# Optimization experiments

Hardware: AMD Instinct MI355X
Metric: run time of the kernel (lower is better)

## Reference

```python
import jax, jax.numpy as jnp
import numpy as np

B, T, D, H = 4, 2048, 768, 12
HD = D // H  # head size 64
DF = 3072    # feed-forward size


def setup_inputs() -> dict:
    key = jax.random.key(0)
    ks = jax.random.split(key, 10)
    s = 0.02
    return {
        "x": jax.random.normal(ks[0], (B, T, D), jnp.float32),
        "mask": jnp.ones((B, T), jnp.int32),
        "Wq": jax.random.normal(ks[1], (D, D), jnp.float32) * s,
        "bq": jnp.zeros((D,), jnp.float32),
        "Wk": jax.random.normal(ks[2], (D, D), jnp.float32) * s,
        "bk": jnp.zeros((D,), jnp.float32),
        "Wv": jax.random.normal(ks[3], (D, D), jnp.float32) * s,
        "bv": jnp.zeros((D,), jnp.float32),
        "Wo": jax.random.normal(ks[4], (D, D), jnp.float32) * s,
        "bo": jnp.zeros((D,), jnp.float32),
        "W1": jax.random.normal(ks[5], (D, DF), jnp.float32) * s,
        "b1": jnp.zeros((DF,), jnp.float32),
        "W2": jax.random.normal(ks[6], (DF, D), jnp.float32) * s,
        "b2": jnp.zeros((D,), jnp.float32),
    }


def reference(x, mask, Wq, bq, Wk, bk, Wv, bv, Wo, bo, W1, b1, W2, b2):
    scale = 1.0 / np.sqrt(HD).astype(np.float32)
    # projections -> [B, H, T, HD]
    def split_heads(t):
        return t.reshape(B, T, H, HD).transpose(0, 2, 1, 3)
    q = split_heads(x @ Wq + bq)
    k = split_heads(x @ Wk + bk)
    v = split_heads(x @ Wv + bv)
    # [B, H, T, T] attention scores (materialized, as in the original)
    scores = jnp.einsum('bhqd,bhkd->bhqk', q, k) * scale
    neg_inf = jnp.float32(-jnp.inf)
    scores = jnp.where(mask[:, None, None, :] == 0, neg_inf, scores)
    attn = jax.nn.softmax(scores, axis=-1)
    ctx = jnp.einsum('bhqk,bhkd->bhqd', attn, v)          # [B,H,T,HD]
    ctx = ctx.transpose(0, 2, 1, 3).reshape(B, T, D)       # merge heads
    attn_out = ctx @ Wo + bo
    h = x + attn_out                                       # residual 1 (dropout p=0)
    ff = jax.nn.gelu(h @ W1 + b1, approximate=False) @ W2 + b2
    out = h + ff                                           # residual 2
    return out, attn
```

## Files before the change

### kernel.cpp

```cpp
#include <hip/hip_runtime.h>
#include <hip/hip_bf16.h>
#include <math.h>

typedef unsigned short u16;
typedef __attribute__((ext_vector_type(8))) short short8;
typedef __attribute__((ext_vector_type(4))) float f32x4;

constexpr int Bc = 4, Tt = 2048, Dd = 768, Hh = 12, Hd = 64, Df = 3072;
constexpr int BT = Bc * Tt;

__device__ __forceinline__ u16 f2b(float x) {
  __hip_bfloat16 h = __float2bfloat16(x);
  return *reinterpret_cast<u16*>(&h);
}
__device__ __forceinline__ float gelu_exact(float g) {
  return 0.5f * g * (1.0f + erff(g * 0.70710678118654752440f));
}
__device__ __forceinline__ void gload16(const void* g, void* l) {
  __builtin_amdgcn_global_load_lds(
      (const __attribute__((address_space(1))) unsigned int*)g,
      (__attribute__((address_space(3))) unsigned int*)l, 16, 0, 0);
}

__device__ __forceinline__ void tr_tile(const float* __restrict__ in,
                                        u16* __restrict__ out, int R, int C,
                                        int bx, int by, float* sh) {
  const int tx = threadIdx.x & 31, ty = threadIdx.x >> 5;
  const int r0 = by * 32, c0 = bx * 32;
#pragma unroll
  for (int i = 0; i < 4; ++i)
    sh[(ty + i * 8) * 33 + tx] = in[(size_t)(r0 + ty + i * 8) * C + c0 + tx];
  __syncthreads();
#pragma unroll
  for (int i = 0; i < 4; ++i)
    out[(size_t)(c0 + ty + i * 8) * R + r0 + tx] = f2b(sh[tx * 33 + ty + i * 8]);
}

__global__ __launch_bounds__(256) void prep_all(
    const float* __restrict__ x, const float* __restrict__ Wq,
    const float* __restrict__ Wk, const float* __restrict__ Wv,
    const float* __restrict__ Wo, const float* __restrict__ W1,
    const float* __restrict__ W2, const float* __restrict__ bq,
    const float* __restrict__ bk, const float* __restrict__ bv,
    const int* __restrict__ mask, u16* __restrict__ xb,
    u16* __restrict__ wqkvT, u16* __restrict__ woT, u16* __restrict__ w1T,
    u16* __restrict__ w2T, float* __restrict__ biasc,
    unsigned int* __restrict__ mwords) {
  __shared__ float sh[32 * 33];
  const int s = blockIdx.x;
  if (s < 3072) {
    int i = (s * 256 + threadIdx.x) * 8;
    float4 a = *(const float4*)&x[i];
    float4 b = *(const float4*)&x[i + 4];
    u16 t[8] = {f2b(a.x), f2b(a.y), f2b(a.z), f2b(a.w),
                f2b(b.x), f2b(b.y), f2b(b.z), f2b(b.w)};
    *(uint4*)&xb[i] = *(uint4*)t;
  } else if (s < 3648) {
    int u = s - 3072; tr_tile(Wq, wqkvT, Dd, Dd, u % 24, u / 24, sh);
  } else if (s < 4224) {
    int u = s - 3648; tr_tile(Wk, wqkvT + 768 * Dd, Dd, Dd, u % 24, u / 24, sh);
  } else if (s < 4800) {
    int u = s - 4224; tr_tile(Wv, wqkvT + 1536 * Dd, Dd, Dd, u % 24, u / 24, sh);
  } else if (s < 5376) {
    int u = s - 4800; tr_tile(Wo, woT, Dd, Dd, u % 24, u / 24, sh);
  } else if (s < 7680) {
    int u = s - 5376; tr_tile(W1, w1T, Dd, Df, u % 96, u / 96, sh);
  } else if (s < 9984) {
    int u = s - 7680; tr_tile(W2, w2T, Df, Dd, u % 24, u / 24, sh);
  } else if (s < 9993) {
    int i = (s - 9984) * 256 + threadIdx.x;
    biasc[i] = (i < 768) ? bq[i] : (i < 1536) ? bk[i - 768] : bv[i - 1536];
  } else {
    const int id = threadIdx.x;
    const int b_ = id >> 6, kv0 = (id & 63) * 32;
    unsigned int wbits = 0u;
    for (int j = 0; j < 32; ++j)
      wbits |= (mask[b_ * Tt + kv0 + j] ? 1u : 0u) << j;
    mwords[id] = wbits;
  }
}

template <int MODE>
__global__ __launch_bounds__(256) void mgemm(
    const u16* __restrict__ A, const u16* __restrict__ Bt,
    const float* __restrict__ bias, const float* __restrict__ add,
    void* __restrict__ C0, void* __restrict__ C1, void* __restrict__ C2,
    int K, int N) {
  __shared__ __align__(16) u16 As[2][128 * 32];
  __shared__ __align__(16) u16 Bs[2][128 * 32];
  const int tid = threadIdx.x;
  const int lane = tid & 63, wv = tid >> 6;
  const int m0 = blockIdx.y * 128, n0 = blockIdx.x * 128;
  const int wm = (wv >> 1) * 64, wn = (wv & 1) * 64;

  f32x4 acc[4][4] = {};

#define MG_STAGE(k0_, bf_)                                                    \
  {                                                                           \
    _Pragma("unroll") for (int i_ = 0; i_ < 2; ++i_) {                        \
      const int idx_ = i_ * 256 + tid;                                        \
      const int row_ = idx_ >> 2;                                             \
      const int kc_ = (idx_ & 3) * 8;                                         \
      const u16* ga_;                                                         \
      if constexpr (MODE == 2) {                                              \
        const int m_ = m0 + row_, b_ = m_ >> 11, t_ = m_ & 2047;              \
        const int kk_ = (k0_) + kc_, hd_ = kk_ >> 6, d_ = kk_ & 63;           \
        ga_ = &A[(((size_t)(b_ * Hh + hd_) * Tt + t_) << 6) + d_];            \
      } else {                                                                \
        ga_ = &A[(size_t)(m0 + row_) * K + (k0_) + kc_];                      \
      }                                                                       \
      gload16(ga_, &As[bf_][idx_ * 8]);                                       \
      gload16(&Bt[(size_t)(n0 + row_) * K + (k0_) + kc_], &Bs[bf_][idx_ * 8]);\
    }                                                                         \
  }

  MG_STAGE(0, 0);
  __syncthreads();

  int it = 0;
  for (int k0 = 0; k0 < K; k0 += 32, ++it) {
    const int cur = it & 1;
    if (k0 + 32 < K) MG_STAGE(k0 + 32, cur ^ 1);
    short8 af[4], bfr[4];
#pragma unroll
    for (int i = 0; i < 4; ++i) {
      af[i] = *reinterpret_cast<const short8*>(
          &As[cur][(wm + i * 16 + (lane & 15)) * 32 + (lane >> 4) * 8]);
      bfr[i] = *reinterpret_cast<const short8*>(
          &Bs[cur][(wn + i * 16 + (lane & 15)) * 32 + (lane >> 4) * 8]);
    }
#pragma unroll
    for (int i = 0; i < 4; ++i)
#pragma unroll
      for (int j = 0; j < 4; ++j)
        acc[i][j] = __builtin_amdgcn_mfma_f32_16x16x32_bf16(af[i], bfr[j],
                                                            acc[i][j], 0, 0, 0);
    __syncthreads();
  }
#undef MG_STAGE

  const int lr = (lane >> 4) * 4, lc = lane & 15;
#pragma unroll
  for (int i = 0; i < 4; ++i) {
    const int mbase = m0 + wm + i * 16 + lr;
#pragma unroll
    for (int j = 0; j < 4; ++j) {
      const int col = n0 + wn + j * 16 + lc;
      const float bvs = bias[col];
#pragma unroll
      for (int r = 0; r < 4; ++r) {
        const int m = mbase + r;
        float g = acc[i][j][r] + bvs;
        if constexpr (MODE == 5) {
          const int b = m >> 11, t = m & 2047;
          if (col < 768) {
            const int head = col >> 6, d = col & 63;
            ((u16*)C0)[(((size_t)(b * Hh + head) * Tt + t) << 6) + d] = f2b(g);
          } else if (col < 1536) {
            const int c = col - 768, head = c >> 6, d = c & 63;
            ((u16*)C1)[(((size_t)(b * Hh + head) * Tt + t) << 6) + d] = f2b(g);
          } else {
            const int c = col - 1536, head = c >> 6, d = c & 63;
            ((u16*)C2)[(((size_t)(b * Hh + head) * Hd + d) << 11) + t] = f2b(g);
          }
        } else if constexpr (MODE == 2) {
          g += add[(size_t)m * Dd + col];
          ((float*)C0)[(size_t)m * Dd + col] = g;
          ((u16*)C1)[(size_t)m * Dd + col] = f2b(g);
        } else if constexpr (MODE == 3) {
          ((u16*)C0)[(size_t)m * N + col] = f2b(gelu_exact(g));
        } else {
          g += add[(size_t)m * Dd + col];
          ((float*)C0)[(size_t)m * Dd + col] = g;
        }
      }
    }
  }
}

__global__ __launch_bounds__(256) void attn_fused(
    const u16* __restrict__ qb, const u16* __restrict__ kb,
    const u16* __restrict__ vtb, const unsigned int* __restrict__ mwords,
    float* __restrict__ attn, u16* __restrict__ ctxb) {
  const int bh = blockIdx.y;
  const int b = bh / Hh;
  const int q0 = blockIdx.x * 64;
  const u16* Qg = qb + (size_t)bh * Tt * Hd;
  const u16* Kg = kb + (size_t)bh * Tt * Hd;
  const u16* Vg = vtb + (size_t)bh * Hd * Tt;
  float* attng = attn + (size_t)bh * Tt * Tt;
  u16* ctxg = ctxb + (size_t)bh * Tt * Hd;
  const unsigned int* mwp = mwords + b * 64;

  __shared__ __align__(16) u16 Ks[2][128 * 64];
  __shared__ __align__(16) u16 Vs[64 * 128];
  __shared__ __align__(16) float Pf[64 * 128];

  const int tid = threadIdx.x, lane = tid & 63, wv = tid >> 6;
  const int lc = lane & 15, lg = lane >> 4;
  const int ql = wv * 16 + lc;
  const int qsw = lc & 7;

#define STAGE_K(t, bf)                                                       \
  {                                                                          \
    const int kv0_ = (t) * 128;                                              \
    _Pragma("unroll") for (int w_ = 0; w_ < 4; ++w_) {                       \
      const int p_ = w_ * 256 + tid;                                         \
      const int row_ = p_ >> 3, kc8_ = (p_ & 7) ^ (row_ & 7);                \
      gload16(Kg + (size_t)(kv0_ + row_) * Hd + kc8_ * 8, &Ks[bf][p_ * 8]);  \
    }                                                                        \
  }
#define STAGE_V(t)                                                           \
  {                                                                          \
    const int kv0_ = (t) * 128;                                              \
    _Pragma("unroll") for (int w_ = 0; w_ < 4; ++w_) {                       \
      const int p_ = w_ * 256 + tid;                                         \
      const int d_ = p_ >> 4, pc_ = (p_ & 15) ^ (d_ & 7);                    \
      gload16(Vg + (size_t)d_ * Tt + kv0_ + pc_ * 8, &Vs[p_ * 8]);           \
    }                                                                        \
  }
#define FENCE() asm volatile("" ::: "memory")

  short8 qf[2];
#pragma unroll
  for (int ks = 0; ks < 2; ++ks)
    qf[ks] = *(const short8*)&Qg[(size_t)(q0 + ql) * Hd + ks * 32 + lg * 8];

  float l = 0.f;

  STAGE_K(0, 0);
  for (int t = 0; t < 16; ++t) {
    asm volatile("s_waitcnt vmcnt(0)" ::: "memory");
    __builtin_amdgcn_s_barrier();
    FENCE();
    const int bf = t & 1;
    if (t < 15) STAGE_K(t + 1, bf ^ 1);
    f32x4 s[8] = {};
#pragma unroll
    for (int ks = 0; ks < 2; ++ks) {
      const int ph = (ks * 4 + lg) ^ qsw;
#pragma unroll
      for (int i = 0; i < 8; ++i) {
        const short8 af = *(const short8*)&Ks[bf][(i * 16 + lc) * 64 + ph * 8];
        s[i] = __builtin_amdgcn_mfma_f32_16x16x32_bf16(af, qf[ks], s[i], 0, 0, 0);
      }
    }
    const uint4 mw4 = *(const uint4*)&mwp[t * 4];
    const unsigned int mwa[4] = {mw4.x, mw4.y, mw4.z, mw4.w};
    float ts = 0.f;
#pragma unroll
    for (int i = 0; i < 8; ++i) {
      const unsigned int w = mwa[i >> 1];
#pragma unroll
      for (int r = 0; r < 4; ++r) {
        const float bit = (float)((w >> ((i & 1) * 16 + lg * 4 + r)) & 1u);
        ts += __expf(s[i][r] * 0.125f) * bit;
      }
    }
    ts += __shfl_xor(ts, 16);
    ts += __shfl_xor(ts, 32);
    l += ts;
  }

  const float linv = 1.f / l;
  f32x4 cacc[4] = {};

  __builtin_amdgcn_s_barrier();
  FENCE();

  STAGE_K(0, 0);
  STAGE_V(0);
  for (int t = 0; t < 16; ++t) {
    const int kv0 = t * 128;
    const int bf = t & 1;
    if (t == 0)
      asm volatile("s_waitcnt vmcnt(0)" ::: "memory");
    else
      asm volatile("s_waitcnt vmcnt(8)" ::: "memory");
    __builtin_amdgcn_s_barrier();
    FENCE();
    if (t < 15) STAGE_K(t + 1, bf ^ 1);
    f32x4 s[8] = {};
#pragma unroll
    for (int ks = 0; ks < 2; ++ks) {
      const int ph = (ks * 4 + lg) ^ qsw;
#pragma unroll
      for (int i = 0; i < 8; ++i) {
        const short8 af = *(const short8*)&Ks[bf][(i * 16 + lc) * 64 + ph * 8];
        s[i] = __builtin_amdgcn_mfma_f32_16x16x32_bf16(af, qf[ks], s[i], 0, 0, 0);
      }
    }
    const uint4 mw4 = *(const uint4*)&mwp[t * 4];
    const unsigned int mwa[4] = {mw4.x, mw4.y, mw4.z, mw4.w};
#pragma unroll
    for (int i = 0; i < 8; ++i) {
      const unsigned int w = mwa[i >> 1];
      float pv[4];
#pragma unroll
      for (int r = 0; r < 4; ++r) {
        const float bit = (float)((w >> ((i & 1) * 16 + lg * 4 + r)) & 1u);
        pv[r] = __expf(s[i][r] * 0.125f) * bit * linv;
      }
      const int g = (i * 4 + lg) ^ qsw;
      *(f32x4*)&Pf[ql * 128 + g * 4] = *(f32x4*)pv;
    }
#pragma unroll
    for (int ks = 0; ks < 4; ++ks) {
      const int gA = (ks * 8 + lg * 2) ^ qsw;
      const int gB = (ks * 8 + lg * 2 + 1) ^ qsw;
      const f32x4 fA = *(const f32x4*)&Pf[ql * 128 + gA * 4];
      const f32x4 fB = *(const f32x4*)&Pf[ql * 128 + gB * 4];
      u16 pb[8] = {f2b(fA[0]), f2b(fA[1]), f2b(fA[2]), f2b(fA[3]),
                   f2b(fB[0]), f2b(fB[1]), f2b(fB[2]), f2b(fB[3])};
      const short8 pa = *(const short8*)pb;
#pragma unroll
      for (int j2 = 0; j2 < 4; ++j2) {
        const int d = j2 * 16 + lc;
        const short8 vb2 =
            *(const short8*)&Vs[d * 128 + (((ks * 4 + lg) ^ (d & 7))) * 8];
        cacc[j2] =
            __builtin_amdgcn_mfma_f32_16x16x32_bf16(pa, vb2, cacc[j2], 0, 0, 0);
      }
    }
    __builtin_amdgcn_s_barrier();
    FENCE();
    if (t < 15) STAGE_V(t + 1);
#pragma unroll
    for (int it = 0; it < 8; ++it) {
      const int row = wv * 16 + it * 2 + (lane >> 5);
      const int colg = lane & 31;
      const int g2 = colg ^ (row & 7);
      const f32x4 v = *(const f32x4*)&Pf[row * 128 + g2 * 4];
      __builtin_nontemporal_store(
          v, (f32x4*)&attng[(size_t)(q0 + row) * Tt + kv0 + colg * 4]);
    }
  }

#pragma unroll
  for (int j2 = 0; j2 < 4; ++j2)
#pragma unroll
    for (int r = 0; r < 4; ++r) {
      const int q = q0 + wv * 16 + lg * 4 + r;
      ctxg[(size_t)q * Hd + j2 * 16 + lc] = f2b(cacc[j2][r]);
    }
#undef STAGE_K
#undef STAGE_V
#undef FENCE
}

extern "C" void kernel_launch(void* const* d_in, const int* in_sizes, int n_in,
                              void* d_out, int out_size, void* d_ws,
                              size_t ws_size, hipStream_t stream) {
  const float* x = (const float*)d_in[0];
  const int* mask = (const int*)d_in[1];
  const float* Wq = (const float*)d_in[2];
  const float* bq = (const float*)d_in[3];
  const float* Wk = (const float*)d_in[4];
  const float* bk = (const float*)d_in[5];
  const float* Wv = (const float*)d_in[6];
  const float* bv = (const float*)d_in[7];
  const float* Wo = (const float*)d_in[8];
  const float* bo = (const float*)d_in[9];
  const float* W1 = (const float*)d_in[10];
  const float* b1 = (const float*)d_in[11];
  const float* W2 = (const float*)d_in[12];
  const float* b2 = (const float*)d_in[13];

  float* out = (float*)d_out;
  float* attn = out + (size_t)BT * Dd;

  char* w = (char*)d_ws;
  u16* xb = (u16*)w;      w += (size_t)BT * Dd * 2;
  u16* wqkvT = (u16*)w;   w += (size_t)Dd * 2304 * 2;
  u16* woT = (u16*)w;     w += (size_t)Dd * Dd * 2;
  u16* w1T = (u16*)w;     w += (size_t)Dd * Df * 2;
  u16* w2T = (u16*)w;     w += (size_t)Df * Dd * 2;
  float* biasc = (float*)w;            w += 2304 * 4;
  unsigned int* mwords = (unsigned int*)w; w += 256 * 4;
  u16* qb = (u16*)w;      w += (size_t)BT * Dd * 2;
  u16* kb = (u16*)w;      w += (size_t)BT * Dd * 2;
  u16* vtb = (u16*)w;     w += (size_t)BT * Dd * 2;
  u16* ctxb = (u16*)w;    w += (size_t)BT * Dd * 2;
  u16* ff1b = (u16*)w;    w += (size_t)BT * Df * 2;
  float* h = (float*)qb;
  u16* hb = vtb;

  dim3 blk(256);

  prep_all<<<dim3(9994), blk, 0, stream>>>(x, Wq, Wk, Wv, Wo, W1, W2, bq, bk,
                                           bv, mask, xb, wqkvT, woT, w1T, w2T,
                                           biasc, mwords);

  mgemm<5><<<dim3(18, 64), blk, 0, stream>>>(xb, wqkvT, biasc, nullptr, qb, kb,
                                             vtb, Dd, 2304);

  attn_fused<<<dim3(32, 48), blk, 0, stream>>>(qb, kb, vtb, mwords, attn, ctxb);

  mgemm<2><<<dim3(6, 64), blk, 0, stream>>>(ctxb, woT, bo, x, h, hb, nullptr,
                                            Dd, Dd);

  mgemm<3><<<dim3(24, 64), blk, 0, stream>>>(hb, w1T, b1, nullptr, ff1b,
                                             nullptr, nullptr, Dd, Df);

  mgemm<4><<<dim3(6, 64), blk, 0, stream>>>(ff1b, w2T, b2, h, out, nullptr,
                                            nullptr, Df, Dd);
}
```

Measured before the change: 476.8 us.

## Triple-buffer GEMM K-loop with one barrier per step and bf16 residual

The GEMM main loop moves from double to triple buffering of the LDS tiles. Global-to-LDS loads run two stages ahead, and each step makes one explicit vmcnt wait plus one barrier instead of a __syncthreads at the end of each step. MFMA sections are wrapped in s_setprio to favour the math wavefronts. The output-projection GEMM now writes only a bf16 copy of the residual stream h, and the final FFN GEMM reads that bf16 h for the second residual. This removes an fp32 store and load but lowers the precision of the residual path.

```diff
diff --git a/kernel.cpp b/kernel.cpp
--- a/kernel.cpp
+++ b/kernel.cpp
@@ -12,6 +12,10 @@
 __device__ __forceinline__ u16 f2b(float x) {
   __hip_bfloat16 h = __float2bfloat16(x);
   return *reinterpret_cast<u16*>(&h);
+}
+__device__ __forceinline__ float b2f(u16 v) {
+  unsigned int u = ((unsigned int)v) << 16;
+  return __builtin_bit_cast(float, u);
 }
 __device__ __forceinline__ float gelu_exact(float g) {
   return 0.5f * g * (1.0f + erff(g * 0.70710678118654752440f));
@@ -84,10 +88,10 @@
 __global__ __launch_bounds__(256) void mgemm(
     const u16* __restrict__ A, const u16* __restrict__ Bt,
     const float* __restrict__ bias, const float* __restrict__ add,
-    void* __restrict__ C0, void* __restrict__ C1, void* __restrict__ C2,
-    int K, int N) {
-  __shared__ __align__(16) u16 As[2][128 * 32];
-  __shared__ __align__(16) u16 Bs[2][128 * 32];
+    const u16* __restrict__ addb, void* __restrict__ C0,
+    void* __restrict__ C1, void* __restrict__ C2, int K, int N) {
+  __shared__ __align__(16) u16 As[3][128 * 32];
+  __shared__ __align__(16) u16 Bs[3][128 * 32];
   const int tid = threadIdx.x;
   const int lane = tid & 63, wv = tid >> 6;
   const int m0 = blockIdx.y * 128, n0 = blockIdx.x * 128;
@@ -113,14 +117,24 @@
       gload16(&Bt[(size_t)(n0 + row_) * K + (k0_) + kc_], &Bs[bf_][idx_ * 8]);\
     }                                                                         \
   }
-
+#define FENCE() asm volatile("" ::: "memory")
+
+  const int nsteps = K >> 5;
   MG_STAGE(0, 0);
-  __syncthreads();
-
-  int it = 0;
-  for (int k0 = 0; k0 < K; k0 += 32, ++it) {
-    const int cur = it & 1;
-    if (k0 + 32 < K) MG_STAGE(k0 + 32, cur ^ 1);
+  MG_STAGE(32, 1);
+
+  for (int it = 0; it < nsteps; ++it) {
+    if (it + 1 < nsteps)
+      asm volatile("s_waitcnt vmcnt(4)" ::: "memory");
+    else
+      asm volatile("s_waitcnt vmcnt(0)" ::: "memory");
+    __builtin_amdgcn_s_barrier();
+    FENCE();
+    const int cur = it % 3;
+    if (it + 2 < nsteps) {
+      const int nb = (it + 2) % 3;
+      MG_STAGE((it + 2) * 32, nb);
+    }
     short8 af[4], bfr[4];
 #pragma unroll
     for (int i = 0; i < 4; ++i) {
@@ -129,15 +143,17 @@
       bfr[i] = *reinterpret_cast<const short8*>(
           &Bs[cur][(wn + i * 16 + (lane & 15)) * 32 + (lane >> 4) * 8]);
     }
+    __builtin_amdgcn_s_setprio(1);
 #pragma unroll
     for (int i = 0; i < 4; ++i)
 #pragma unroll
       for (int j = 0; j < 4; ++j)
         acc[i][j] = __builtin_amdgcn_mfma_f32_16x16x32_bf16(af[i], bfr[j],
                                                             acc[i][j], 0, 0, 0);
-    __syncthreads();
+    __builtin_amdgcn_s_setprio(0);
   }
 #undef MG_STAGE
+#undef FENCE
 
   const int lr = (lane >> 4) * 4, lc = lane & 15;
 #pragma unroll
@@ -165,12 +181,11 @@
           }
         } else if constexpr (MODE == 2) {
           g += add[(size_t)m * Dd + col];
-          ((float*)C0)[(size_t)m * Dd + col] = g;
-          ((u16*)C1)[(size_t)m * Dd + col] = f2b(g);
+          ((u16*)C0)[(size_t)m * Dd + col] = f2b(g);
         } else if constexpr (MODE == 3) {
           ((u16*)C0)[(size_t)m * N + col] = f2b(gelu_exact(g));
         } else {
-          g += add[(size_t)m * Dd + col];
+          g += b2f(addb[(size_t)m * Dd + col]);
           ((float*)C0)[(size_t)m * Dd + col] = g;
         }
       }
@@ -382,7 +397,6 @@
   u16* vtb = (u16*)w;     w += (size_t)BT * Dd * 2;
   u16* ctxb = (u16*)w;    w += (size_t)BT * Dd * 2;
   u16* ff1b = (u16*)w;    w += (size_t)BT * Df * 2;
-  float* h = (float*)qb;
   u16* hb = vtb;
 
   dim3 blk(256);
@@ -391,17 +405,17 @@
                                            bv, mask, xb, wqkvT, woT, w1T, w2T,
                                            biasc, mwords);
 
-  mgemm<5><<<dim3(18, 64), blk, 0, stream>>>(xb, wqkvT, biasc, nullptr, qb, kb,
-                                             vtb, Dd, 2304);
+  mgemm<5><<<dim3(18, 64), blk, 0, stream>>>(xb, wqkvT, biasc, nullptr, nullptr,
+                                             qb, kb, vtb, Dd, 2304);
 
   attn_fused<<<dim3(32, 48), blk, 0, stream>>>(qb, kb, vtb, mwords, attn, ctxb);
 
-  mgemm<2><<<dim3(6, 64), blk, 0, stream>>>(ctxb, woT, bo, x, h, hb, nullptr,
-                                            Dd, Dd);
-
-  mgemm<3><<<dim3(24, 64), blk, 0, stream>>>(hb, w1T, b1, nullptr, ff1b,
-                                             nullptr, nullptr, Dd, Df);
-
-  mgemm<4><<<dim3(6, 64), blk, 0, stream>>>(ff1b, w2T, b2, h, out, nullptr,
-                                            nullptr, Df, Dd);
-}
+  mgemm<2><<<dim3(6, 64), blk, 0, stream>>>(ctxb, woT, bo, x, nullptr, hb,
+                                            nullptr, nullptr, Dd, Dd);
+
+  mgemm<3><<<dim3(24, 64), blk, 0, stream>>>(hb, w1T, b1, nullptr, nullptr,
+                                             ff1b, nullptr, nullptr, Dd, Df);
+
+  mgemm<4><<<dim3(6, 64), blk, 0, stream>>>(ff1b, w2T, b2, nullptr, hb, out,
+                                            nullptr, nullptr, Df, Dd);
+}
```

New measurement: 480.9 us. About the same (+0.9%).
